# Optimization experiments

Hardware: AMD Instinct MI355X
Metric: run time of the kernel (lower is better)

## Reference

```python
import jax, jax.numpy as jnp
import numpy as np

B, CH1, CH2, HID, T, E = 64, 3, 4, 16, 16384, 512

def setup_inputs() -> dict:
    key = jax.random.key(0)
    ks = jax.random.split(key, 12)
    s_t = 1.0 / np.sqrt(T)   # fan_in = input_dim for q/k/v projections
    s_e = 1.0 / np.sqrt(E)   # fan_in = embed_dim for out_proj
    return {
        "x":  jax.random.normal(ks[0], (B, 7, T), jnp.float32),
        "W1": jax.random.normal(ks[1], (HID, CH1), jnp.float32) / np.sqrt(CH1),
        "W2": jax.random.normal(ks[2], (HID, CH2), jnp.float32) / np.sqrt(CH2),
        "Wq": jax.random.normal(ks[3], (E, T), jnp.float32) * s_t,
        "bq": jnp.zeros((E,), jnp.float32),
        "Wk": jax.random.normal(ks[4], (E, T), jnp.float32) * s_t,
        "bk": jnp.zeros((E,), jnp.float32),
        "Wv": jax.random.normal(ks[5], (E, T), jnp.float32) * s_t,
        "bv": jnp.zeros((E,), jnp.float32),
        "Wo": jax.random.normal(ks[6], (T, E), jnp.float32) * s_e,
        "bo": jnp.zeros((T,), jnp.float32),
        "W3": jax.random.normal(ks[7], (CH1, HID), jnp.float32) / np.sqrt(HID),
    }

def reference(x, W1, W2, Wq, bq, Wk, bk, Wv, bv, Wo, bo, W3):
    p = x[:, :CH1]            # [B,3,T]  narrow(1,0,ch_1)
    c = x[:, 3:3 + CH2]       # [B,4,T]  narrow(1,3,ch_2)
    q = jnp.einsum('oc,bct->bot', W1, p)   # fc_1: [B,16,T]
    cc = jnp.einsum('oc,bct->bot', W2, c)  # fc_2: [B,16,T]
    # CrossAttention: Linears act on last dim (T -> E)
    Q = jnp.einsum('bct,et->bce', q, Wq) + bq    # [B,16,E]
    K = jnp.einsum('bct,et->bce', cc, Wk) + bk   # [B,16,E]
    V = jnp.einsum('bct,et->bce', cc, Wv) + bv   # [B,16,E]
    scale = 1.0 / np.sqrt(HID)                   # nch = 16 query channels
    attn_w = jax.nn.softmax(jnp.einsum('bce,bcf->bef', Q, K) * scale, axis=-1)  # [B,E,E]
    attn = jnp.einsum('bef,bcf->bce', attn_w, V)  # [B,16,E]
    out = jnp.einsum('bce,te->bct', attn, Wo) + bo  # out_proj: [B,16,T]
    y = jnp.einsum('oc,bct->bot', W3, out)          # fc_3: [B,3,T]
    return p + y
```

## Files before the change

kernel.cpp:

```cpp
#include <hip/hip_runtime.h>

#define BB 64
#define TT 16384
#define EE 512

typedef _Float16 half8 __attribute__((ext_vector_type(8)));
typedef float floatx4 __attribute__((ext_vector_type(4)));

static __device__ __forceinline__ half8 cvt_half8(float4 a, float4 b) {
  half8 h;
  h[0] = (_Float16)a.x; h[1] = (_Float16)a.y; h[2] = (_Float16)a.z; h[3] = (_Float16)a.w;
  h[4] = (_Float16)b.x; h[5] = (_Float16)b.y; h[6] = (_Float16)b.z; h[7] = (_Float16)b.w;
  return h;
}

__global__ __launch_bounds__(256) void zero_ws(float4* __restrict__ p) {
  p[blockIdx.x * 256 + threadIdx.x] = (float4){0.f, 0.f, 0.f, 0.f};
}

__global__ __launch_bounds__(256) void proj_gemm(
    const float* __restrict__ x, const float* __restrict__ Wq,
    const float* __restrict__ Wk, const float* __restrict__ Wv,
    float* __restrict__ Xq, float* __restrict__ Xkv)
{
  __shared__ _Float16 As[64][40];
  __shared__ _Float16 Bs[128][40];
  const int t = threadIdx.x;
  const int wave = t >> 6, lane = t & 63;
  const int quad = lane >> 4, l16 = lane & 15;

  const int tile = blockIdx.x;
  int mtile, ntile, chan_base, cpb, ldout;
  const float *Wa, *Wb;
  float* outC;
  if (tile < 12) {
    mtile = tile >> 2; ntile = tile & 3;
    chan_base = 0; cpb = 3; ldout = 512;
    Wa = Wq; Wb = Wq; outC = Xq;
  } else {
    const int t2 = tile - 12;
    mtile = t2 >> 3; ntile = t2 & 7;
    chan_base = 3; cpb = 4; ldout = 1024;
    Wa = Wk; Wb = Wv; outC = Xkv;
  }
  const int k0 = blockIdx.y << 9;

  const int arow = t >> 2, akk = (t & 3) << 3;
  const int r = mtile * 64 + arow;
  const int bidx = r / cpb;
  const int j = r - bidx * cpb;
  const float* aptr = x + (size_t)(bidx * 7 + chan_base + j) * TT + k0 + akk;

  const int brow = t >> 1, bkk = (t & 1) << 4;
  const int ncol = ntile * 128 + brow;
  const float* wsrc = (ncol < EE) ? Wa : Wb;
  const float* bptr = wsrc + (size_t)(ncol & (EE - 1)) * TT + k0 + bkk;

  floatx4 acc[4][2];
  for (int rt = 0; rt < 4; ++rt)
    for (int ct = 0; ct < 2; ++ct)
      acc[rt][ct] = (floatx4){0.f, 0.f, 0.f, 0.f};

  float4 a0 = *(const float4*)aptr;
  float4 a1 = *(const float4*)(aptr + 4);
  float4 b0 = *(const float4*)bptr;
  float4 b1 = *(const float4*)(bptr + 4);
  float4 b2 = *(const float4*)(bptr + 8);
  float4 b3 = *(const float4*)(bptr + 12);

  for (int kt = 0; kt < 16; ++kt) {
    const half8 ha  = cvt_half8(a0, a1);
    const half8 hb0 = cvt_half8(b0, b1);
    const half8 hb1 = cvt_half8(b2, b3);
    __syncthreads();
    *(half8*)&As[arow][akk]     = ha;
    *(half8*)&Bs[brow][bkk]     = hb0;
    *(half8*)&Bs[brow][bkk + 8] = hb1;
    __syncthreads();
    if (kt < 15) {
      aptr += 32; bptr += 32;
      a0 = *(const float4*)aptr;
      a1 = *(const float4*)(aptr + 4);
      b0 = *(const float4*)bptr;
      b1 = *(const float4*)(bptr + 4);
      b2 = *(const float4*)(bptr + 8);
      b3 = *(const float4*)(bptr + 12);
    }
    half8 bf0 = *(const half8*)&Bs[wave * 32 + l16][quad * 8];
    half8 bf1 = *(const half8*)&Bs[wave * 32 + 16 + l16][quad * 8];
#pragma unroll
    for (int rt = 0; rt < 4; ++rt) {
      half8 af = *(const half8*)&As[rt * 16 + l16][quad * 8];
      acc[rt][0] = __builtin_amdgcn_mfma_f32_16x16x32_f16(af, bf0, acc[rt][0], 0, 0, 0);
      acc[rt][1] = __builtin_amdgcn_mfma_f32_16x16x32_f16(af, bf1, acc[rt][1], 0, 0, 0);
    }
  }
#pragma unroll
  for (int rt = 0; rt < 4; ++rt) {
#pragma unroll
    for (int ct = 0; ct < 2; ++ct) {
      const int gr = mtile * 64 + rt * 16 + quad * 4;
      const int gc = ntile * 128 + wave * 32 + ct * 16 + l16;
#pragma unroll
      for (int rg = 0; rg < 4; ++rg)
        atomicAdd(&outC[(size_t)(gr + rg) * ldout + gc], acc[rt][ct][rg]);
    }
  }
}

__global__ __launch_bounds__(256) void attn_mid(
    const float* __restrict__ Xq, const float* __restrict__ Xkv,
    const float* __restrict__ W1, const float* __restrict__ W2,
    const float* __restrict__ W3,
    const float* __restrict__ bq, const float* __restrict__ bk,
    const float* __restrict__ bv, _Float16* __restrict__ U)
{
  __shared__ float Ks[16][512];
  __shared__ float VW[3][512];
  __shared__ float Qs[16][64];
  __shared__ float Xs[4][512];
  __shared__ float W1s[48], W2s[64], W3s[48], W32s[12], w3sum[3];
  const int t = threadIdx.x;
  const int b = blockIdx.y;
  const int e0 = blockIdx.x * 64;

  if (t < 48) W1s[t] = W1[t];
  if (t >= 64 && t < 128) W2s[t - 64] = W2[t - 64];
  if (t >= 128 && t < 176) W3s[t - 128] = W3[t - 128];
  __syncthreads();
  if (t < 12) {
    const int o = t >> 2, jj = t & 3;
    float s = 0.f;
    for (int c = 0; c < 16; ++c) s += W3s[o * 16 + c] * W2s[c * 4 + jj];
    W32s[t] = s;
  }
  if (t >= 16 && t < 19) {
    const int o = t - 16;
    float s = 0.f;
    for (int c = 0; c < 16; ++c) s += W3s[o * 16 + c];
    w3sum[o] = s;
  }
  for (int i = t; i < 2048; i += 256) {
    const int jj = i >> 9, f = i & 511;
    Xs[jj][f] = Xkv[(size_t)(b * 4 + jj) * 1024 + f];
  }
  __syncthreads();
  for (int i = t; i < 8192; i += 256) {
    const int c = i >> 9, f = i & 511;
    float s = bk[f];
#pragma unroll
    for (int jj = 0; jj < 4; ++jj) s += W2s[c * 4 + jj] * Xs[jj][f];
    Ks[c][f] = s;
  }
  __syncthreads();
  for (int i = t; i < 2048; i += 256) {
    const int jj = i >> 9, f = i & 511;
    Xs[jj][f] = Xkv[(size_t)(b * 4 + jj) * 1024 + 512 + f];
  }
  __syncthreads();
  for (int i = t; i < 1536; i += 256) {
    const int o = i >> 9, f = i & 511;
    float s = w3sum[o] * bv[f];
#pragma unroll
    for (int jj = 0; jj < 4; ++jj) s += W32s[o * 4 + jj] * Xs[jj][f];
    VW[o][f] = s;
  }
  for (int i = t; i < 1024; i += 256) {
    const int c = i >> 6, el = i & 63;
    float s = bq[e0 + el];
#pragma unroll
    for (int jj = 0; jj < 3; ++jj)
      s += W1s[c * 3 + jj] * Xq[(size_t)(b * 3 + jj) * 512 + e0 + el];
    Qs[c][el] = s;
  }
  __syncthreads();

  const int wave = t >> 6, lane = t & 63;
  float vwr[3][8];
#pragma unroll
  for (int o = 0; o < 3; ++o) {
    float4 va = *(const float4*)&VW[o][lane * 8];
    float4 vb = *(const float4*)&VW[o][lane * 8 + 4];
    vwr[o][0] = va.x; vwr[o][1] = va.y; vwr[o][2] = va.z; vwr[o][3] = va.w;
    vwr[o][4] = vb.x; vwr[o][5] = vb.y; vwr[o][6] = vb.z; vwr[o][7] = vb.w;
  }

  for (int g = 0; g < 4; ++g) {
    const int el0 = wave * 16 + g * 4;
    float s[4][8];
#pragma unroll
    for (int e = 0; e < 4; ++e)
#pragma unroll
      for (int i = 0; i < 8; ++i) s[e][i] = 0.f;
#pragma unroll
    for (int c = 0; c < 16; ++c) {
      float4 k0 = *(const float4*)&Ks[c][lane * 8];
      float4 k1 = *(const float4*)&Ks[c][lane * 8 + 4];
      float4 qv = *(const float4*)&Qs[c][el0];
      float qa[4] = {qv.x, qv.y, qv.z, qv.w};
#pragma unroll
      for (int e = 0; e < 4; ++e) {
        const float q = qa[e];
        s[e][0] += q * k0.x; s[e][1] += q * k0.y; s[e][2] += q * k0.z; s[e][3] += q * k0.w;
        s[e][4] += q * k1.x; s[e][5] += q * k1.y; s[e][6] += q * k1.z; s[e][7] += q * k1.w;
      }
    }
#pragma unroll
    for (int e = 0; e < 4; ++e) {
      float mx = s[e][0];
#pragma unroll
      for (int i = 1; i < 8; ++i) mx = fmaxf(mx, s[e][i]);
#pragma unroll
      for (int off = 32; off; off >>= 1) mx = fmaxf(mx, __shfl_xor(mx, off));
      float p[8], sum = 0.f;
#pragma unroll
      for (int i = 0; i < 8; ++i) { p[i] = __expf(0.25f * (s[e][i] - mx)); sum += p[i]; }
      float u0 = 0.f, u1 = 0.f, u2 = 0.f;
#pragma unroll
      for (int i = 0; i < 8; ++i) {
        u0 += p[i] * vwr[0][i];
        u1 += p[i] * vwr[1][i];
        u2 += p[i] * vwr[2][i];
      }
#pragma unroll
      for (int off = 32; off; off >>= 1) {
        sum += __shfl_xor(sum, off);
        u0  += __shfl_xor(u0, off);
        u1  += __shfl_xor(u1, off);
        u2  += __shfl_xor(u2, off);
      }
      if (lane == 0) {
        const float inv = 1.0f / sum;
        const size_t base = (size_t)b * 3 * 512 + (e0 + el0 + e);
        U[base]        = (_Float16)(u0 * inv);
        U[base + 512]  = (_Float16)(u1 * inv);
        U[base + 1024] = (_Float16)(u2 * inv);
      }
    }
  }
}

__global__ __launch_bounds__(256) void out_gemm(
    const _Float16* __restrict__ U, const float* __restrict__ Wo,
    const float* __restrict__ x, const float* __restrict__ bo,
    const float* __restrict__ W3, float* __restrict__ outY)
{
  __shared__ _Float16 As[64][40];
  __shared__ _Float16 Bs[64][40];
  __shared__ float w3sh[3];
  const int t = threadIdx.x;
  const int wave = t >> 6, lane = t & 63;
  const int quad = lane >> 4, l16 = lane & 15;
  const int mtile = blockIdx.y, ntile = blockIdx.x;
  if (t < 3) {
    float s = 0.f;
    for (int c = 0; c < 16; ++c) s += W3[t * 16 + c];
    w3sh[t] = s;
  }
  const int arow = t >> 2, akk = (t & 3) << 3;
  const _Float16* aptr = U + (size_t)(mtile * 64 + arow) * EE + akk;
  const int brow = t >> 2, bkk = (t & 3) << 3;
  const float* bptr = Wo + (size_t)(ntile * 64 + brow) * EE + bkk;

  floatx4 acc[4];
  for (int rt = 0; rt < 4; ++rt) acc[rt] = (floatx4){0.f, 0.f, 0.f, 0.f};

  half8 av = *(const half8*)aptr;
  float4 b0 = *(const float4*)bptr;
  float4 b1 = *(const float4*)(bptr + 4);

  for (int kt = 0; kt < 16; ++kt) {
    const half8 hb = cvt_half8(b0, b1);
    const half8 ha = av;
    __syncthreads();
    *(half8*)&As[arow][akk] = ha;
    *(half8*)&Bs[brow][bkk] = hb;
    __syncthreads();
    if (kt < 15) {
      aptr += 32; bptr += 32;
      av = *(const half8*)aptr;
      b0 = *(const float4*)bptr;
      b1 = *(const float4*)(bptr + 4);
    }
    half8 bf = *(const half8*)&Bs[wave * 16 + l16][quad * 8];
#pragma unroll
    for (int rt = 0; rt < 4; ++rt) {
      half8 af = *(const half8*)&As[rt * 16 + l16][quad * 8];
      acc[rt] = __builtin_amdgcn_mfma_f32_16x16x32_f16(af, bf, acc[rt], 0, 0, 0);
    }
  }
#pragma unroll
  for (int rt = 0; rt < 4; ++rt) {
    const int gr = mtile * 64 + rt * 16 + quad * 4;
    const int tc = ntile * 64 + wave * 16 + l16;
    const float bot = bo[tc];
#pragma unroll
    for (int rg = 0; rg < 4; ++rg) {
      const int rr = gr + rg;
      const int bb = rr / 3, oo = rr - bb * 3;
      const float v = acc[rt][rg]
                    + x[(size_t)(bb * 7 + oo) * TT + tc]
                    + w3sh[oo] * bot;
      outY[(size_t)rr * TT + tc] = v;
    }
  }
}

extern "C" void kernel_launch(void* const* d_in, const int* in_sizes, int n_in,
                              void* d_out, int out_size, void* d_ws, size_t ws_size,
                              hipStream_t stream) {
  const float* x  = (const float*)d_in[0];
  const float* W1 = (const float*)d_in[1];
  const float* W2 = (const float*)d_in[2];
  const float* Wq = (const float*)d_in[3];
  const float* bq = (const float*)d_in[4];
  const float* Wk = (const float*)d_in[5];
  const float* bk = (const float*)d_in[6];
  const float* Wv = (const float*)d_in[7];
  const float* bv = (const float*)d_in[8];
  const float* Wo = (const float*)d_in[9];
  const float* bo = (const float*)d_in[10];
  const float* W3 = (const float*)d_in[11];
  float* out = (float*)d_out;

  char* ws = (char*)d_ws;
  float* Xq      = (float*)ws;
  float* Xkv     = (float*)(ws + 393216);
  _Float16* U    = (_Float16*)(ws + 1441792);

  zero_ws<<<dim3(352), 256, 0, stream>>>((float4*)ws);

  proj_gemm<<<dim3(44, 32), 256, 0, stream>>>(x, Wq, Wk, Wv, Xq, Xkv);
  attn_mid<<<dim3(8, BB), 256, 0, stream>>>(Xq, Xkv, W1, W2, W3, bq, bk, bv, U);
  out_gemm<<<dim3(256, 3), 256, 0, stream>>>(U, Wo, x, bo, W3, out);
}
```

Baseline: 274.1 us.

## Double-buffer LDS tiles and shrink GEMM tiles for more blocks

Both projection and output GEMMs now use double-buffered shared-memory tiles with a single barrier per k-step, so the fp16 staging of the next tile overlaps the MFMA work on the current one. Tiles are halved: proj_gemm goes from 64x128 to 64x64 (twice the blocks), and out_gemm goes from 64x64 to 64x32 with a 2x2 wave layout and a swapped grid order. The aim is more parallelism and latency hiding on these memory-bound GEMMs. The costs are more atomics and re-reads of the A operand in proj_gemm, and fewer MFMAs per block.

```diff
diff --git a/kernel.cpp b/kernel.cpp
--- a/kernel.cpp
+++ b/kernel.cpp
@@ -5,6 +5,7 @@
 #define EE 512
 
 typedef _Float16 half8 __attribute__((ext_vector_type(8)));
+typedef _Float16 half4 __attribute__((ext_vector_type(4)));
 typedef float floatx4 __attribute__((ext_vector_type(4)));
 
 static __device__ __forceinline__ half8 cvt_half8(float4 a, float4 b) {
@@ -13,6 +14,11 @@
   h[4] = (_Float16)b.x; h[5] = (_Float16)b.y; h[6] = (_Float16)b.z; h[7] = (_Float16)b.w;
   return h;
 }
+static __device__ __forceinline__ half4 cvt_half4(float4 a) {
+  half4 h;
+  h[0] = (_Float16)a.x; h[1] = (_Float16)a.y; h[2] = (_Float16)a.z; h[3] = (_Float16)a.w;
+  return h;
+}
 
 __global__ __launch_bounds__(256) void zero_ws(float4* __restrict__ p) {
   p[blockIdx.x * 256 + threadIdx.x] = (float4){0.f, 0.f, 0.f, 0.f};
@@ -23,8 +29,8 @@
     const float* __restrict__ Wk, const float* __restrict__ Wv,
     float* __restrict__ Xq, float* __restrict__ Xkv)
 {
-  __shared__ _Float16 As[64][40];
-  __shared__ _Float16 Bs[128][40];
+  __shared__ _Float16 As[2][64][40];
+  __shared__ _Float16 Bs[2][64][40];
   const int t = threadIdx.x;
   const int wave = t >> 6, lane = t & 63;
   const int quad = lane >> 4, l16 = lane & 15;
@@ -33,13 +39,13 @@
   int mtile, ntile, chan_base, cpb, ldout;
   const float *Wa, *Wb;
   float* outC;
-  if (tile < 12) {
-    mtile = tile >> 2; ntile = tile & 3;
+  if (tile < 24) {
+    mtile = tile >> 3; ntile = tile & 7;
     chan_base = 0; cpb = 3; ldout = 512;
     Wa = Wq; Wb = Wq; outC = Xq;
   } else {
-    const int t2 = tile - 12;
-    mtile = t2 >> 3; ntile = t2 & 7;
+    const int t2 = tile - 24;
+    mtile = t2 >> 4; ntile = t2 & 15;
     chan_base = 3; cpb = 4; ldout = 1024;
     Wa = Wk; Wb = Wv; outC = Xkv;
   }
@@ -51,60 +57,50 @@
   const int j = r - bidx * cpb;
   const float* aptr = x + (size_t)(bidx * 7 + chan_base + j) * TT + k0 + akk;
 
-  const int brow = t >> 1, bkk = (t & 1) << 4;
-  const int ncol = ntile * 128 + brow;
+  const int brow = t >> 2, bkk = (t & 3) << 3;
+  const int ncol = ntile * 64 + brow;
   const float* wsrc = (ncol < EE) ? Wa : Wb;
   const float* bptr = wsrc + (size_t)(ncol & (EE - 1)) * TT + k0 + bkk;
 
-  floatx4 acc[4][2];
-  for (int rt = 0; rt < 4; ++rt)
-    for (int ct = 0; ct < 2; ++ct)
-      acc[rt][ct] = (floatx4){0.f, 0.f, 0.f, 0.f};
-
-  float4 a0 = *(const float4*)aptr;
-  float4 a1 = *(const float4*)(aptr + 4);
-  float4 b0 = *(const float4*)bptr;
-  float4 b1 = *(const float4*)(bptr + 4);
-  float4 b2 = *(const float4*)(bptr + 8);
-  float4 b3 = *(const float4*)(bptr + 12);
+  floatx4 acc[4];
+#pragma unroll
+  for (int rt = 0; rt < 4; ++rt) acc[rt] = (floatx4){0.f, 0.f, 0.f, 0.f};
+
+  float4 a0 = *(const float4*)aptr, a1 = *(const float4*)(aptr + 4);
+  float4 b0 = *(const float4*)bptr, b1 = *(const float4*)(bptr + 4);
+  *(half8*)&As[0][arow][akk] = cvt_half8(a0, a1);
+  *(half8*)&Bs[0][brow][bkk] = cvt_half8(b0, b1);
+  aptr += 32; bptr += 32;
+  a0 = *(const float4*)aptr; a1 = *(const float4*)(aptr + 4);
+  b0 = *(const float4*)bptr; b1 = *(const float4*)(bptr + 4);
+  __syncthreads();
 
   for (int kt = 0; kt < 16; ++kt) {
-    const half8 ha  = cvt_half8(a0, a1);
-    const half8 hb0 = cvt_half8(b0, b1);
-    const half8 hb1 = cvt_half8(b2, b3);
+    const int p = kt & 1;
+    half8 bf = *(const half8*)&Bs[p][wave * 16 + l16][quad * 8];
+#pragma unroll
+    for (int rt = 0; rt < 4; ++rt) {
+      half8 af = *(const half8*)&As[p][rt * 16 + l16][quad * 8];
+      acc[rt] = __builtin_amdgcn_mfma_f32_16x16x32_f16(af, bf, acc[rt], 0, 0, 0);
+    }
+    if (kt < 15) {
+      *(half8*)&As[1 - p][arow][akk] = cvt_half8(a0, a1);
+      *(half8*)&Bs[1 - p][brow][bkk] = cvt_half8(b0, b1);
+    }
+    if (kt < 14) {
+      aptr += 32; bptr += 32;
+      a0 = *(const float4*)aptr; a1 = *(const float4*)(aptr + 4);
+      b0 = *(const float4*)bptr; b1 = *(const float4*)(bptr + 4);
+    }
     __syncthreads();
-    *(half8*)&As[arow][akk]     = ha;
-    *(half8*)&Bs[brow][bkk]     = hb0;
-    *(half8*)&Bs[brow][bkk + 8] = hb1;
-    __syncthreads();
-    if (kt < 15) {
-      aptr += 32; bptr += 32;
-      a0 = *(const float4*)aptr;
-      a1 = *(const float4*)(aptr + 4);
-      b0 = *(const float4*)bptr;
-      b1 = *(const float4*)(bptr + 4);
-      b2 = *(const float4*)(bptr + 8);
-      b3 = *(const float4*)(bptr + 12);
-    }
-    half8 bf0 = *(const half8*)&Bs[wave * 32 + l16][quad * 8];
-    half8 bf1 = *(const half8*)&Bs[wave * 32 + 16 + l16][quad * 8];
-#pragma unroll
-    for (int rt = 0; rt < 4; ++rt) {
-      half8 af = *(const half8*)&As[rt * 16 + l16][quad * 8];
-      acc[rt][0] = __builtin_amdgcn_mfma_f32_16x16x32_f16(af, bf0, acc[rt][0], 0, 0, 0);
-      acc[rt][1] = __builtin_amdgcn_mfma_f32_16x16x32_f16(af, bf1, acc[rt][1], 0, 0, 0);
-    }
   }
 #pragma unroll
   for (int rt = 0; rt < 4; ++rt) {
-#pragma unroll
-    for (int ct = 0; ct < 2; ++ct) {
-      const int gr = mtile * 64 + rt * 16 + quad * 4;
-      const int gc = ntile * 128 + wave * 32 + ct * 16 + l16;
-#pragma unroll
-      for (int rg = 0; rg < 4; ++rg)
-        atomicAdd(&outC[(size_t)(gr + rg) * ldout + gc], acc[rt][ct][rg]);
-    }
+    const int gr = mtile * 64 + rt * 16 + quad * 4;
+    const int gc = ntile * 64 + wave * 16 + l16;
+#pragma unroll
+    for (int rg = 0; rg < 4; ++rg)
+      atomicAdd(&outC[(size_t)(gr + rg) * ldout + gc], acc[rt][rg]);
   }
 }
 
@@ -245,13 +241,14 @@
     const float* __restrict__ x, const float* __restrict__ bo,
     const float* __restrict__ W3, float* __restrict__ outY)
 {
-  __shared__ _Float16 As[64][40];
-  __shared__ _Float16 Bs[64][40];
+  __shared__ _Float16 As[2][64][40];
+  __shared__ _Float16 Bs[2][32][40];
   __shared__ float w3sh[3];
   const int t = threadIdx.x;
   const int wave = t >> 6, lane = t & 63;
   const int quad = lane >> 4, l16 = lane & 15;
-  const int mtile = blockIdx.y, ntile = blockIdx.x;
+  const int mw = wave & 1, nw = wave >> 1;
+  const int mtile = blockIdx.x, ntile = blockIdx.y;
   if (t < 3) {
     float s = 0.f;
     for (int c = 0; c < 16; ++c) s += W3[t * 16 + c];
@@ -259,40 +256,45 @@
   }
   const int arow = t >> 2, akk = (t & 3) << 3;
   const _Float16* aptr = U + (size_t)(mtile * 64 + arow) * EE + akk;
-  const int brow = t >> 2, bkk = (t & 3) << 3;
-  const float* bptr = Wo + (size_t)(ntile * 64 + brow) * EE + bkk;
-
-  floatx4 acc[4];
-  for (int rt = 0; rt < 4; ++rt) acc[rt] = (floatx4){0.f, 0.f, 0.f, 0.f};
+  const int brow = t >> 3, bkk = (t & 7) << 2;
+  const float* bptr = Wo + (size_t)(ntile * 32 + brow) * EE + bkk;
+
+  floatx4 acc[2];
+  acc[0] = (floatx4){0.f, 0.f, 0.f, 0.f};
+  acc[1] = (floatx4){0.f, 0.f, 0.f, 0.f};
 
   half8 av = *(const half8*)aptr;
-  float4 b0 = *(const float4*)bptr;
-  float4 b1 = *(const float4*)(bptr + 4);
+  float4 bv4 = *(const float4*)bptr;
+  *(half8*)&As[0][arow][akk] = av;
+  *(half4*)&Bs[0][brow][bkk] = cvt_half4(bv4);
+  aptr += 32; bptr += 32;
+  av = *(const half8*)aptr;
+  bv4 = *(const float4*)bptr;
+  __syncthreads();
 
   for (int kt = 0; kt < 16; ++kt) {
-    const half8 hb = cvt_half8(b0, b1);
-    const half8 ha = av;
-    __syncthreads();
-    *(half8*)&As[arow][akk] = ha;
-    *(half8*)&Bs[brow][bkk] = hb;
-    __syncthreads();
+    const int p = kt & 1;
+    half8 bf = *(const half8*)&Bs[p][nw * 16 + l16][quad * 8];
+#pragma unroll
+    for (int rt = 0; rt < 2; ++rt) {
+      half8 af = *(const half8*)&As[p][mw * 32 + rt * 16 + l16][quad * 8];
+      acc[rt] = __builtin_amdgcn_mfma_f32_16x16x32_f16(af, bf, acc[rt], 0, 0, 0);
+    }
     if (kt < 15) {
+      *(half8*)&As[1 - p][arow][akk] = av;
+      *(half4*)&Bs[1 - p][brow][bkk] = cvt_half4(bv4);
+    }
+    if (kt < 14) {
       aptr += 32; bptr += 32;
       av = *(const half8*)aptr;
-      b0 = *(const float4*)bptr;
-      b1 = *(const float4*)(bptr + 4);
-    }
-    half8 bf = *(const half8*)&Bs[wave * 16 + l16][quad * 8];
-#pragma unroll
-    for (int rt = 0; rt < 4; ++rt) {
-      half8 af = *(const half8*)&As[rt * 16 + l16][quad * 8];
-      acc[rt] = __builtin_amdgcn_mfma_f32_16x16x32_f16(af, bf, acc[rt], 0, 0, 0);
-    }
-  }
-#pragma unroll
-  for (int rt = 0; rt < 4; ++rt) {
-    const int gr = mtile * 64 + rt * 16 + quad * 4;
-    const int tc = ntile * 64 + wave * 16 + l16;
+      bv4 = *(const float4*)bptr;
+    }
+    __syncthreads();
+  }
+#pragma unroll
+  for (int rt = 0; rt < 2; ++rt) {
+    const int gr = mtile * 64 + mw * 32 + rt * 16 + quad * 4;
+    const int tc = ntile * 32 + nw * 16 + l16;
     const float bot = bo[tc];
 #pragma unroll
     for (int rg = 0; rg < 4; ++rg) {
@@ -330,7 +332,7 @@
 
   zero_ws<<<dim3(352), 256, 0, stream>>>((float4*)ws);
 
-  proj_gemm<<<dim3(44, 32), 256, 0, stream>>>(x, Wq, Wk, Wv, Xq, Xkv);
+  proj_gemm<<<dim3(88, 32), 256, 0, stream>>>(x, Wq, Wk, Wv, Xq, Xkv);
   attn_mid<<<dim3(8, BB), 256, 0, stream>>>(Xq, Xkv, W1, W2, W3, bq, bk, bv, U);
-  out_gemm<<<dim3(256, 3), 256, 0, stream>>>(U, Wo, x, bo, W3, out);
-}
+  out_gemm<<<dim3(3, 512), 256, 0, stream>>>(U, Wo, x, bo, W3, out);
+}
```

New measurement: 277.5 us. Within noise of the previous version (+1.2%).
